# Kernel optimization log

Measured on AMD Instinct MI355X. Metric: run time of the kernel, lower is better.

## Reference

```python
import jax, jax.numpy as jnp
import numpy as np

D, E, K, H = 512, 8, 2, 128   # input_dim, num_experts, top-k, expert hidden (Expert default)
CAPF = 1.25                    # capacity_factor
N = 32768                      # tokens


def setup_inputs() -> dict:
    key = jax.random.key(0)
    ks = jax.random.split(key, 6)
    s = 0.02
    return {
        "x":  jax.random.normal(ks[0], (N, D), jnp.float32),
        "Wr": jax.random.normal(ks[1], (D, E), jnp.float32) * s,   # router linear weight
        "br": jnp.zeros((E,), jnp.float32),
        "W1": jax.random.normal(ks[2], (E, D, H), jnp.float32) * s,  # expert first linear (stacked)
        "b1": jnp.zeros((E, H), jnp.float32),
        "W2": jax.random.normal(ks[3], (E, H, D), jnp.float32) * s,  # expert second linear (stacked)
        "b2": jnp.zeros((E, D), jnp.float32),
    }


def reference(x, Wr, br, W1, b1, W2, b2):
    n = x.shape[0]
    # ---- router (eval mode: no noise, temperature=1) ----
    logits = x @ Wr + br                                   # [N, E]
    topk_vals, topk_idx = jax.lax.top_k(logits, K)         # [N, K]
    gates_k = jax.nn.softmax(topk_vals, axis=-1)
    rows = jnp.arange(n)[:, None]
    sparse_gates = jnp.zeros_like(logits).at[rows, topk_idx].set(gates_k)  # [N, E]
    confidence = topk_vals.max(axis=-1).mean()
    # ---- capacity-limited dispatch (keep first `cap` routed tokens per expert) ----
    cap = int(CAPF * (n / E))
    mask = sparse_gates > 0                                # [N, E] routed mask
    pos = jnp.cumsum(mask, axis=0) - 1                     # rank of token within expert queue
    keep = mask & (pos < cap)                              # [N, E]
    load = keep.sum(axis=0).astype(x.dtype)                # [E]
    # ---- per-expert 2-layer FFN over all tokens, combined with keep mask ----
    # (original adds expert output un-weighted by gates to kept token positions)
    h = jax.nn.relu(jnp.einsum('nd,edh->enh', x, W1) + b1[:, None, :])   # [E, N, H]
    y = jnp.einsum('enh,ehd->end', h, W2) + b2[:, None, :]               # [E, N, D]
    out = jnp.einsum('ne,end->nd', keep.astype(x.dtype), y)             # [N, D]
    # ---- load-balance stats ----
    load_dist = load / (load.sum() + 1e-8)
    load_loss = (load_dist * jnp.log(load_dist + 1e-8)).sum()
    return out, load_loss, load_dist, confidence
```

## Files before the change

### kernel.cpp

```cpp
#include <hip/hip_runtime.h>

#define D 512
#define E 8
#define H 128
#define BM 64
#define HP 136
#define RT 16

typedef __attribute__((ext_vector_type(8))) short short8v;
typedef __attribute__((ext_vector_type(4))) short short4v;
typedef __attribute__((ext_vector_type(4))) float float4v;

__device__ inline short f2bf(float f) {
  union { float f; unsigned u; } v; v.f = f;
  unsigned r = v.u + 0x7fffu + ((v.u >> 16) & 1u);
  return (short)(r >> 16);
}
__device__ inline float bf2f(short s) {
  union { unsigned u; float f; } v;
  v.u = ((unsigned)(unsigned short)s) << 16;
  return v.f;
}
__device__ inline void gload_lds4(const void* g, void* l) {
  __builtin_amdgcn_global_load_lds(
      (const __attribute__((address_space(1))) unsigned int*)g,
      (__attribute__((address_space(3))) unsigned int*)l, 4, 0, 0);
}

__global__ void k_swizzle(const float* __restrict__ W1, const float* __restrict__ W2,
                          short* __restrict__ W1f, short* __restrict__ W2f) {
  const int e = blockIdx.y;
  const int lane = threadIdx.x & 63;
  const int wv = threadIdx.x >> 6;
  const int r = lane & 15, g = lane >> 4;
  const int which = blockIdx.x >> 4;
  const int fbase = ((blockIdx.x & 15) * 4 + wv) * 2;
  if (which == 0) {
#pragma unroll
    for (int f = fbase; f < fbase + 2; ++f) {
      int ks = f >> 3, t = f & 7;
      const float* src = W1 + ((size_t)e * D + ks * 32 + g * 8) * H + t * 16 + r;
      short8v o;
#pragma unroll
      for (int j = 0; j < 8; ++j) o[j] = f2bf(src[(size_t)j * H]);
      *(short8v*)(W1f + (((size_t)e * 128 + f) * 64 + lane) * 8) = o;
    }
  } else {
#pragma unroll
    for (int f = fbase; f < fbase + 2; ++f) {
      int t = f >> 2, ks = f & 3;
      const float* src = W2 + ((size_t)e * H + ks * 32 + g * 8) * D + t * 16 + r;
      short8v o;
#pragma unroll
      for (int j = 0; j < 8; ++j) o[j] = f2bf(src[(size_t)j * D]);
      *(short8v*)(W2f + (((size_t)e * 128 + f) * 64 + lane) * 8) = o;
    }
  }
}

__global__ void k_router(const float* __restrict__ x, const float* __restrict__ Wr,
                         const float* __restrict__ br, int* __restrict__ tokE,
                         float* __restrict__ confPart, short* __restrict__ xb) {
  const int lane = threadIdx.x & 63;
  const int wave = threadIdx.x >> 6;
  const int tbase = (blockIdx.x * 4 + wave) * RT;

  float wr[8][8];
  const float4* wrp = reinterpret_cast<const float4*>(Wr) + lane * 16;
#pragma unroll
  for (int j = 0; j < 8; ++j) {
    float4 a = wrp[j * 2 + 0];
    float4 b = wrp[j * 2 + 1];
    wr[j][0] = a.x; wr[j][1] = a.y; wr[j][2] = a.z; wr[j][3] = a.w;
    wr[j][4] = b.x; wr[j][5] = b.y; wr[j][6] = b.z; wr[j][7] = b.w;
  }

  const int myE = ((lane & 1) << 2) | (lane & 2) | ((lane >> 2) & 1);
  const float brv = br[myE];

  float conf = 0.f;

#pragma unroll 2
  for (int tt = 0; tt < RT; ++tt) {
    const int token = tbase + tt;
    const float4* xp = reinterpret_cast<const float4*>(x + (size_t)token * D + lane * 8);
    float4 x0 = xp[0], x1 = xp[1];
    float xv[8] = {x0.x, x0.y, x0.z, x0.w, x1.x, x1.y, x1.z, x1.w};

    if (xb) {
      short8v p;
#pragma unroll
      for (int j = 0; j < 8; ++j) p[j] = f2bf(xv[j]);
      *(short8v*)(xb + (size_t)token * D + lane * 8) = p;
    }

    float v[8] = {0, 0, 0, 0, 0, 0, 0, 0};
#pragma unroll
    for (int j = 0; j < 8; ++j)
#pragma unroll
      for (int e = 0; e < E; ++e)
        v[e] += xv[j] * wr[j][e];

#pragma unroll
    for (int i = 0; i < 4; ++i) {
      float a = v[i] + __shfl_xor(v[i], 1, 64);
      float b = v[i + 4] + __shfl_xor(v[i + 4], 1, 64);
      v[i] = (lane & 1) ? b : a;
    }
#pragma unroll
    for (int i = 0; i < 2; ++i) {
      float a = v[i] + __shfl_xor(v[i], 2, 64);
      float b = v[i + 2] + __shfl_xor(v[i + 2], 2, 64);
      v[i] = (lane & 2) ? b : a;
    }
    {
      float a = v[0] + __shfl_xor(v[0], 4, 64);
      float b = v[1] + __shfl_xor(v[1], 4, 64);
      v[0] = (lane & 4) ? b : a;
    }
    v[0] += __shfl_xor(v[0], 8, 64);
    v[0] += __shfl_xor(v[0], 16, 64);
    v[0] += __shfl_xor(v[0], 32, 64);

    const float logit = v[0] + brv;

    float m1 = logit; int i1 = myE;
#pragma unroll
    for (int m = 1; m <= 4; m <<= 1) {
      float om = __shfl_xor(m1, m, 64);
      int oi = __shfl_xor(i1, m, 64);
      bool take = (om > m1) || (om == m1 && oi < i1);
      m1 = take ? om : m1;
      i1 = take ? oi : i1;
    }
    float s1 = (myE == i1) ? -1e30f : logit; int j1 = myE;
#pragma unroll
    for (int m = 1; m <= 4; m <<= 1) {
      float om = __shfl_xor(s1, m, 64);
      int oi = __shfl_xor(j1, m, 64);
      bool take = (om > s1) || (om == s1 && oi < j1);
      s1 = take ? om : s1;
      j1 = take ? oi : j1;
    }

    if (lane == 0) {
      tokE[token * 2 + 0] = i1;
      tokE[token * 2 + 1] = j1;
    }
    conf += m1;
  }

  __shared__ float cf[4];
  if (lane == 0) cf[wave] = conf;
  __syncthreads();
  if (threadIdx.x == 0) confPart[blockIdx.x] = cf[0] + cf[1] + cf[2] + cf[3];
}

__global__ void k_count(const int* __restrict__ tokE, int* __restrict__ chunkCnt) {
  __shared__ int c[E];
  if (threadIdx.x < E) c[threadIdx.x] = 0;
  __syncthreads();
  int token = blockIdx.x * 256 + threadIdx.x;
  atomicAdd(&c[tokE[token * 2 + 0]], 1);
  atomicAdd(&c[tokE[token * 2 + 1]], 1);
  __syncthreads();
  if (threadIdx.x < E) chunkCnt[blockIdx.x * E + threadIdx.x] = c[threadIdx.x];
}

__global__ void k_scan(const int* __restrict__ chunkCnt, const float* __restrict__ confPart,
                       int* __restrict__ chunkOff, int* __restrict__ kept,
                       float* __restrict__ outTail, int nConf, int cap, int nTok) {
  const int lane = threadIdx.x & 63;
  const int e = threadIdx.x >> 6;
  __shared__ int keptS[E];

  int v0 = chunkCnt[lane * E + e];
  int v1 = chunkCnt[(64 + lane) * E + e];
  int s0 = v0, s1 = v1;
#pragma unroll
  for (int off = 1; off < 64; off <<= 1) {
    int t0 = __shfl_up(s0, off, 64);
    int t1 = __shfl_up(s1, off, 64);
    if (lane >= off) { s0 += t0; s1 += t1; }
  }
  int tot0 = __shfl(s0, 63, 64);
  int total = tot0 + __shfl(s1, 63, 64);
  chunkOff[lane * E + e] = s0 - v0;
  chunkOff[(64 + lane) * E + e] = tot0 + s1 - v1;
  if (lane == 0) {
    int k = min(total, cap);
    kept[e] = k;
    keptS[e] = k;
  }

  __shared__ float s[512];
  float a = 0.f;
  for (int i = threadIdx.x; i < nConf; i += 512) a += confPart[i];
  s[threadIdx.x] = a;
  __syncthreads();
  for (int st = 256; st > 0; st >>= 1) {
    if (threadIdx.x < st) s[threadIdx.x] += s[threadIdx.x + st];
    __syncthreads();
  }
  if (threadIdx.x == 0) {
    float tot = 0.f, ld[E];
    for (int i = 0; i < E; ++i) { ld[i] = (float)keptS[i]; tot += ld[i]; }
    float denom = tot + 1e-8f;
    float loss = 0.f;
    for (int i = 0; i < E; ++i) {
      float dist = ld[i] / denom;
      loss += dist * logf(dist + 1e-8f);
      outTail[1 + i] = dist;
    }
    outTail[0] = loss;
    outTail[1 + E] = s[0] / (float)nTok;
  }
}

__global__ void k_dispatch(const int* __restrict__ tokE, const int* __restrict__ chunkOff,
                           int* __restrict__ expList, int2* __restrict__ tokSlot, int cap) {
  const int lane = threadIdx.x & 63;
  const int wave = threadIdx.x >> 6;
  const int token = blockIdx.x * 256 + threadIdx.x;
  const int e0 = tokE[token * 2 + 0];
  const int e1 = tokE[token * 2 + 1];
  __shared__ int wcnt[4][E];
  unsigned long long lt = (lane == 63) ? 0x7fffffffffffffffull : ((1ull << lane) - 1ull);
  int r0 = 0, r1 = 0;
#pragma unroll
  for (int e = 0; e < E; ++e) {
    unsigned long long b0 = __ballot(e0 == e);
    unsigned long long b1 = __ballot(e1 == e);
    unsigned long long m = b0 | b1;
    if (e0 == e) r0 = __popcll(m & lt);
    if (e1 == e) r1 = __popcll(m & lt);
    if (lane == 0) wcnt[wave][e] = __popcll(m);
  }
  __syncthreads();
  int base0 = chunkOff[blockIdx.x * E + e0];
  int base1 = chunkOff[blockIdx.x * E + e1];
  for (int w = 0; w < wave; ++w) {
    base0 += wcnt[w][e0];
    base1 += wcnt[w][e1];
  }
  int g0 = base0 + r0;
  int g1 = base1 + r1;
  if (g0 < cap) expList[e0 * cap + g0] = token;
  if (g1 < cap) expList[e1 * cap + g1] = token;
  tokSlot[token] = make_int2(g0 < cap ? e0 * cap + g0 : -1,
                             g1 < cap ? e1 * cap + g1 : -1);
}

template <bool USE_XB>
__global__ __launch_bounds__(512) void k_expert_mfma(
    const short* __restrict__ xb, const float* __restrict__ x,
    const short* __restrict__ W1f, const float* __restrict__ b1,
    const short* __restrict__ W2f, const float* __restrict__ b2,
    const int* __restrict__ expList, const int* __restrict__ kept,
    short* __restrict__ yscr, int cap) {
  const int e = blockIdx.y;
  const int cnt = kept[e];
  const int t0 = blockIdx.x * BM;
  if (t0 >= cnt) return;
  const int lane = threadIdx.x & 63;
  const int wave = threadIdx.x >> 6;
  const int rowg = wave >> 1;
  const int ng = wave & 1;
  const int rb = rowg * 16;
  const int n15 = lane & 15;
  const int grp = lane >> 4;
  const int kg = grp * 8;

  __shared__ int toks[BM];
  __shared__ short sbuf[2 * BM * HP];

  if (threadIdx.x < BM) {
    int idx = min(t0 + (int)threadIdx.x, cnt - 1);
    toks[threadIdx.x] = expList[e * cap + idx];
  }
  __syncthreads();

  const short* w1 = W1f + (size_t)e * (128 * 512);
  const short* w2 = W2f + (size_t)e * (128 * 512);

  float4v acc[4];
#pragma unroll
  for (int t = 0; t < 4; ++t) acc[t] = (float4v){0.f, 0.f, 0.f, 0.f};

  if (USE_XB) {
    auto stageX = [&](int p) {
#pragma unroll
      for (int j = 0; j < 8; ++j) {
        int ti = wave * 8 + j;
        const short* src = xb + (size_t)toks[ti] * D + p * 128 + lane * 2;
        short* dst = &sbuf[(p & 1) * (BM * HP) + ti * HP];
        gload_lds4(src, dst);
      }
    };
    stageX(0);
    __syncthreads();
#pragma unroll
    for (int p = 0; p < 4; ++p) {
      if (p < 3) stageX(p + 1);
#pragma unroll
      for (int ksl = 0; ksl < 4; ++ksl) {
        const int ks = p * 4 + ksl;
        short8v xf = *(const short8v*)&sbuf[(p & 1) * (BM * HP) +
                                            (rb + n15) * HP + ksl * 32 + kg];
        short8v wf[4];
#pragma unroll
        for (int t = 0; t < 4; ++t)
          wf[t] = *(const short8v*)(w1 + (size_t)(ks * 8 + ng * 4 + t) * 512 + lane * 8);
#pragma unroll
        for (int t = 0; t < 4; ++t)
          acc[t] = __builtin_amdgcn_mfma_f32_16x16x32_bf16(wf[t], xf, acc[t], 0, 0, 0);
      }
      __syncthreads();
    }
  } else {
    const float* xrowF = x + (size_t)toks[rb + n15] * D + kg;
    short8v xf[16];
#pragma unroll
    for (int ks = 0; ks < 16; ++ks) {
      float4 a = *(const float4*)(xrowF + ks * 32);
      float4 b = *(const float4*)(xrowF + ks * 32 + 4);
      short8v f;
      f[0] = f2bf(a.x); f[1] = f2bf(a.y); f[2] = f2bf(a.z); f[3] = f2bf(a.w);
      f[4] = f2bf(b.x); f[5] = f2bf(b.y); f[6] = f2bf(b.z); f[7] = f2bf(b.w);
      xf[ks] = f;
    }
#pragma unroll
    for (int ks = 0; ks < 16; ++ks) {
      short8v wf[4];
#pragma unroll
      for (int t = 0; t < 4; ++t)
        wf[t] = *(const short8v*)(w1 + (size_t)(ks * 8 + ng * 4 + t) * 512 + lane * 8);
#pragma unroll
      for (int t = 0; t < 4; ++t)
        acc[t] = __builtin_amdgcn_mfma_f32_16x16x32_bf16(wf[t], xf[ks], acc[t], 0, 0, 0);
    }
    __syncthreads();
  }

  short* hrow = &sbuf[(rb + n15) * HP];
#pragma unroll
  for (int t = 0; t < 4; ++t) {
    int tg = ng * 4 + t;
    float4 bb = *(const float4*)(b1 + e * H + tg * 16 + grp * 4);
    short4v p;
    p[0] = f2bf(fmaxf(acc[t][0] + bb.x, 0.f));
    p[1] = f2bf(fmaxf(acc[t][1] + bb.y, 0.f));
    p[2] = f2bf(fmaxf(acc[t][2] + bb.z, 0.f));
    p[3] = f2bf(fmaxf(acc[t][3] + bb.w, 0.f));
    *(short4v*)(hrow + tg * 16 + grp * 4) = p;
  }
  __syncthreads();

  short8v a4[4];
#pragma unroll
  for (int ks = 0; ks < 4; ++ks)
    a4[ks] = *(const short8v*)(&sbuf[(rb + n15) * HP + ks * 32 + kg]);

  short* yrow = yscr + ((size_t)(e * cap + t0 + rb + n15)) * D;
#pragma unroll 4
  for (int tt = 0; tt < 16; ++tt) {
    const int t = ng * 16 + tt;
    short8v wf[4];
#pragma unroll
    for (int ks = 0; ks < 4; ++ks)
      wf[ks] = *(const short8v*)(w2 + (size_t)(t * 4 + ks) * 512 + lane * 8);
    float4v y = (float4v){0.f, 0.f, 0.f, 0.f};
#pragma unroll
    for (int ks = 0; ks < 4; ++ks)
      y = __builtin_amdgcn_mfma_f32_16x16x32_bf16(wf[ks], a4[ks], y, 0, 0, 0);
    float4 bb = *(const float4*)(b2 + e * D + t * 16 + grp * 4);
    short4v p;
    p[0] = f2bf(y[0] + bb.x);
    p[1] = f2bf(y[1] + bb.y);
    p[2] = f2bf(y[2] + bb.z);
    p[3] = f2bf(y[3] + bb.w);
    *(short4v*)(yrow + t * 16 + grp * 4) = p;
  }
}

__global__ void k_combine(const short* __restrict__ yscr, const int2* __restrict__ tokSlot,
                          float* __restrict__ out) {
  const int idx = blockIdx.x * 256 + threadIdx.x;
  const int token = idx >> 7;
  const int c4 = idx & 127;
  int2 sl = tokSlot[token];
  float4 r = make_float4(0.f, 0.f, 0.f, 0.f);
  if (sl.x >= 0) {
    short4v y = *(const short4v*)(yscr + (size_t)sl.x * D + c4 * 4);
    r.x += bf2f(y[0]); r.y += bf2f(y[1]); r.z += bf2f(y[2]); r.w += bf2f(y[3]);
  }
  if (sl.y >= 0) {
    short4v y = *(const short4v*)(yscr + (size_t)sl.y * D + c4 * 4);
    r.x += bf2f(y[0]); r.y += bf2f(y[1]); r.z += bf2f(y[2]); r.w += bf2f(y[3]);
  }
  reinterpret_cast<float4*>(out)[idx] = r;
}

extern "C" void kernel_launch(void* const* d_in, const int* in_sizes, int n_in,
                              void* d_out, int out_size, void* d_ws, size_t ws_size,
                              hipStream_t stream) {
  const float* x  = (const float*)d_in[0];
  const float* Wr = (const float*)d_in[1];
  const float* br = (const float*)d_in[2];
  const float* W1 = (const float*)d_in[3];
  const float* b1 = (const float*)d_in[4];
  const float* W2 = (const float*)d_in[5];
  const float* b2 = (const float*)d_in[6];
  float* out = (float*)d_out;

  const int N = in_sizes[0] / D;
  const int cap = (int)(1.25f * (float)(N / E));
  const int chunks = N / 256;
  const int rblocks = N / (4 * RT);

  int* tokE = (int*)d_ws;
  float* confPart = (float*)(tokE + (size_t)N * 2);
  int* chunkCnt = (int*)(confPart + rblocks);
  int* chunkOff = chunkCnt + chunks * E;
  int* kept = chunkOff + chunks * E;
  int2* tokSlot = (int2*)(kept + E);
  int* expList = (int*)(tokSlot + N);
  short* W1f = (short*)(expList + (size_t)E * cap);
  short* W2f = W1f + (size_t)E * H * D;
  short* yscr = W2f + (size_t)E * H * D;
  short* xb = yscr + (size_t)E * cap * D;

  const size_t needed = (size_t)((char*)(xb + (size_t)N * D) - (char*)d_ws);
  const bool useXB = ws_size >= needed;

  k_swizzle<<<dim3(32, E), 256, 0, stream>>>(W1, W2, W1f, W2f);

  k_router<<<rblocks, 256, 0, stream>>>(x, Wr, br, tokE, confPart,
                                        useXB ? xb : nullptr);
  k_count<<<chunks, 256, 0, stream>>>(tokE, chunkCnt);
  k_scan<<<1, 512, 0, stream>>>(chunkCnt, confPart, chunkOff, kept,
                                out + (size_t)N * D, rblocks, cap, N);
  k_dispatch<<<chunks, 256, 0, stream>>>(tokE, chunkOff, expList, tokSlot, cap);

  const int tiles = (cap + BM - 1) / BM;
  dim3 g5(tiles, E);
  if (useXB)
    k_expert_mfma<true><<<g5, 512, 0, stream>>>(xb, x, W1f, b1, W2f, b2,
                                                expList, kept, yscr, cap);
  else
    k_expert_mfma<false><<<g5, 512, 0, stream>>>(nullptr, x, W1f, b1, W2f, b2,
                                                 expList, kept, yscr, cap);

  k_combine<<<(N * D / 4) / 256, 256, 0, stream>>>(yscr, tokSlot, out);
}
```

Before: 111.0 us.

## Double token tile per block so each wave reuses expert weights across two row groups

Raises the expert-kernel token tile from 64 to 128 rows. Each wave now computes two 16-row MFMA tiles that share the same loaded W1/W2 fragments, halving weight traffic per token. Launch bounds pin one block per SM, and LDS use and register pressure roughly double. Fewer blocks are launched, which risks lower occupancy and worse load balance across CUs. Partial tiles at the end of each expert also waste more work.

```diff
diff --git a/kernel.cpp b/kernel.cpp
--- a/kernel.cpp
+++ b/kernel.cpp
@@ -3,7 +3,7 @@
 #define D 512
 #define E 8
 #define H 128
-#define BM 64
+#define BM 128
 #define HP 136
 #define RT 16
 
@@ -252,7 +252,7 @@
 }
 
 template <bool USE_XB>
-__global__ __launch_bounds__(512) void k_expert_mfma(
+__global__ __launch_bounds__(512, 1) void k_expert_mfma(
     const short* __restrict__ xb, const float* __restrict__ x,
     const short* __restrict__ W1f, const float* __restrict__ b1,
     const short* __restrict__ W2f, const float* __restrict__ b2,
@@ -266,7 +266,8 @@
   const int wave = threadIdx.x >> 6;
   const int rowg = wave >> 1;
   const int ng = wave & 1;
-  const int rb = rowg * 16;
+  const int rbA = rowg * 32;
+  const int rbB = rowg * 32 + 16;
   const int n15 = lane & 15;
   const int grp = lane >> 4;
   const int kg = grp * 8;
@@ -283,15 +284,18 @@
   const short* w1 = W1f + (size_t)e * (128 * 512);
   const short* w2 = W2f + (size_t)e * (128 * 512);
 
-  float4v acc[4];
-#pragma unroll
-  for (int t = 0; t < 4; ++t) acc[t] = (float4v){0.f, 0.f, 0.f, 0.f};
+  float4v accA[4], accB[4];
+#pragma unroll
+  for (int t = 0; t < 4; ++t) {
+    accA[t] = (float4v){0.f, 0.f, 0.f, 0.f};
+    accB[t] = (float4v){0.f, 0.f, 0.f, 0.f};
+  }
 
   if (USE_XB) {
     auto stageX = [&](int p) {
 #pragma unroll
-      for (int j = 0; j < 8; ++j) {
-        int ti = wave * 8 + j;
+      for (int j = 0; j < 16; ++j) {
+        int ti = wave * 16 + j;
         const short* src = xb + (size_t)toks[ti] * D + p * 128 + lane * 2;
         short* dst = &sbuf[(p & 1) * (BM * HP) + ti * HP];
         gload_lds4(src, dst);
@@ -305,63 +309,77 @@
 #pragma unroll
       for (int ksl = 0; ksl < 4; ++ksl) {
         const int ks = p * 4 + ksl;
-        short8v xf = *(const short8v*)&sbuf[(p & 1) * (BM * HP) +
-                                            (rb + n15) * HP + ksl * 32 + kg];
+        const short* sb = &sbuf[(p & 1) * (BM * HP)];
+        short8v xfA = *(const short8v*)&sb[(rbA + n15) * HP + ksl * 32 + kg];
+        short8v xfB = *(const short8v*)&sb[(rbB + n15) * HP + ksl * 32 + kg];
         short8v wf[4];
 #pragma unroll
         for (int t = 0; t < 4; ++t)
           wf[t] = *(const short8v*)(w1 + (size_t)(ks * 8 + ng * 4 + t) * 512 + lane * 8);
 #pragma unroll
-        for (int t = 0; t < 4; ++t)
-          acc[t] = __builtin_amdgcn_mfma_f32_16x16x32_bf16(wf[t], xf, acc[t], 0, 0, 0);
+        for (int t = 0; t < 4; ++t) {
+          accA[t] = __builtin_amdgcn_mfma_f32_16x16x32_bf16(wf[t], xfA, accA[t], 0, 0, 0);
+          accB[t] = __builtin_amdgcn_mfma_f32_16x16x32_bf16(wf[t], xfB, accB[t], 0, 0, 0);
+        }
       }
       __syncthreads();
     }
   } else {
-    const float* xrowF = x + (size_t)toks[rb + n15] * D + kg;
-    short8v xf[16];
+    const float* xrowA = x + (size_t)toks[rbA + n15] * D + kg;
+    const float* xrowB = x + (size_t)toks[rbB + n15] * D + kg;
 #pragma unroll
     for (int ks = 0; ks < 16; ++ks) {
-      float4 a = *(const float4*)(xrowF + ks * 32);
-      float4 b = *(const float4*)(xrowF + ks * 32 + 4);
-      short8v f;
-      f[0] = f2bf(a.x); f[1] = f2bf(a.y); f[2] = f2bf(a.z); f[3] = f2bf(a.w);
-      f[4] = f2bf(b.x); f[5] = f2bf(b.y); f[6] = f2bf(b.z); f[7] = f2bf(b.w);
-      xf[ks] = f;
-    }
-#pragma unroll
-    for (int ks = 0; ks < 16; ++ks) {
+      float4 a0 = *(const float4*)(xrowA + ks * 32);
+      float4 a1 = *(const float4*)(xrowA + ks * 32 + 4);
+      float4 b0 = *(const float4*)(xrowB + ks * 32);
+      float4 b1v = *(const float4*)(xrowB + ks * 32 + 4);
+      short8v xfA, xfB;
+      xfA[0] = f2bf(a0.x); xfA[1] = f2bf(a0.y); xfA[2] = f2bf(a0.z); xfA[3] = f2bf(a0.w);
+      xfA[4] = f2bf(a1.x); xfA[5] = f2bf(a1.y); xfA[6] = f2bf(a1.z); xfA[7] = f2bf(a1.w);
+      xfB[0] = f2bf(b0.x); xfB[1] = f2bf(b0.y); xfB[2] = f2bf(b0.z); xfB[3] = f2bf(b0.w);
+      xfB[4] = f2bf(b1v.x); xfB[5] = f2bf(b1v.y); xfB[6] = f2bf(b1v.z); xfB[7] = f2bf(b1v.w);
       short8v wf[4];
 #pragma unroll
       for (int t = 0; t < 4; ++t)
         wf[t] = *(const short8v*)(w1 + (size_t)(ks * 8 + ng * 4 + t) * 512 + lane * 8);
 #pragma unroll
-      for (int t = 0; t < 4; ++t)
-        acc[t] = __builtin_amdgcn_mfma_f32_16x16x32_bf16(wf[t], xf[ks], acc[t], 0, 0, 0);
+      for (int t = 0; t < 4; ++t) {
+        accA[t] = __builtin_amdgcn_mfma_f32_16x16x32_bf16(wf[t], xfA, accA[t], 0, 0, 0);
+        accB[t] = __builtin_amdgcn_mfma_f32_16x16x32_bf16(wf[t], xfB, accB[t], 0, 0, 0);
+      }
     }
     __syncthreads();
   }
 
-  short* hrow = &sbuf[(rb + n15) * HP];
+  short* hrowA = &sbuf[(rbA + n15) * HP];
+  short* hrowB = &sbuf[(rbB + n15) * HP];
 #pragma unroll
   for (int t = 0; t < 4; ++t) {
     int tg = ng * 4 + t;
     float4 bb = *(const float4*)(b1 + e * H + tg * 16 + grp * 4);
-    short4v p;
-    p[0] = f2bf(fmaxf(acc[t][0] + bb.x, 0.f));
-    p[1] = f2bf(fmaxf(acc[t][1] + bb.y, 0.f));
-    p[2] = f2bf(fmaxf(acc[t][2] + bb.z, 0.f));
-    p[3] = f2bf(fmaxf(acc[t][3] + bb.w, 0.f));
-    *(short4v*)(hrow + tg * 16 + grp * 4) = p;
-  }
-  __syncthreads();
-
-  short8v a4[4];
-#pragma unroll
-  for (int ks = 0; ks < 4; ++ks)
-    a4[ks] = *(const short8v*)(&sbuf[(rb + n15) * HP + ks * 32 + kg]);
-
-  short* yrow = yscr + ((size_t)(e * cap + t0 + rb + n15)) * D;
+    short4v pA, pB;
+    pA[0] = f2bf(fmaxf(accA[t][0] + bb.x, 0.f));
+    pA[1] = f2bf(fmaxf(accA[t][1] + bb.y, 0.f));
+    pA[2] = f2bf(fmaxf(accA[t][2] + bb.z, 0.f));
+    pA[3] = f2bf(fmaxf(accA[t][3] + bb.w, 0.f));
+    pB[0] = f2bf(fmaxf(accB[t][0] + bb.x, 0.f));
+    pB[1] = f2bf(fmaxf(accB[t][1] + bb.y, 0.f));
+    pB[2] = f2bf(fmaxf(accB[t][2] + bb.z, 0.f));
+    pB[3] = f2bf(fmaxf(accB[t][3] + bb.w, 0.f));
+    *(short4v*)(hrowA + tg * 16 + grp * 4) = pA;
+    *(short4v*)(hrowB + tg * 16 + grp * 4) = pB;
+  }
+  __syncthreads();
+
+  short8v a4A[4], a4B[4];
+#pragma unroll
+  for (int ks = 0; ks < 4; ++ks) {
+    a4A[ks] = *(const short8v*)(&sbuf[(rbA + n15) * HP + ks * 32 + kg]);
+    a4B[ks] = *(const short8v*)(&sbuf[(rbB + n15) * HP + ks * 32 + kg]);
+  }
+
+  short* yrowA = yscr + ((size_t)(e * cap + t0 + rbA + n15)) * D;
+  short* yrowB = yscr + ((size_t)(e * cap + t0 + rbB + n15)) * D;
 #pragma unroll 4
   for (int tt = 0; tt < 16; ++tt) {
     const int t = ng * 16 + tt;
@@ -369,17 +387,25 @@
 #pragma unroll
     for (int ks = 0; ks < 4; ++ks)
       wf[ks] = *(const short8v*)(w2 + (size_t)(t * 4 + ks) * 512 + lane * 8);
-    float4v y = (float4v){0.f, 0.f, 0.f, 0.f};
-#pragma unroll
-    for (int ks = 0; ks < 4; ++ks)
-      y = __builtin_amdgcn_mfma_f32_16x16x32_bf16(wf[ks], a4[ks], y, 0, 0, 0);
+    float4v yA = (float4v){0.f, 0.f, 0.f, 0.f};
+    float4v yB = (float4v){0.f, 0.f, 0.f, 0.f};
+#pragma unroll
+    for (int ks = 0; ks < 4; ++ks) {
+      yA = __builtin_amdgcn_mfma_f32_16x16x32_bf16(wf[ks], a4A[ks], yA, 0, 0, 0);
+      yB = __builtin_amdgcn_mfma_f32_16x16x32_bf16(wf[ks], a4B[ks], yB, 0, 0, 0);
+    }
     float4 bb = *(const float4*)(b2 + e * D + t * 16 + grp * 4);
-    short4v p;
-    p[0] = f2bf(y[0] + bb.x);
-    p[1] = f2bf(y[1] + bb.y);
-    p[2] = f2bf(y[2] + bb.z);
-    p[3] = f2bf(y[3] + bb.w);
-    *(short4v*)(yrow + t * 16 + grp * 4) = p;
+    short4v pA, pB;
+    pA[0] = f2bf(yA[0] + bb.x);
+    pA[1] = f2bf(yA[1] + bb.y);
+    pA[2] = f2bf(yA[2] + bb.z);
+    pA[3] = f2bf(yA[3] + bb.w);
+    pB[0] = f2bf(yB[0] + bb.x);
+    pB[1] = f2bf(yB[1] + bb.y);
+    pB[2] = f2bf(yB[2] + bb.z);
+    pB[3] = f2bf(yB[3] + bb.w);
+    *(short4v*)(yrowA + t * 16 + grp * 4) = pA;
+    *(short4v*)(yrowB + t * 16 + grp * 4) = pB;
   }
 }
 
```

Measured after the change: 106.8 us. 1.04x faster.
